# Performance work log

Hardware: AMD Instinct MI355X
Metric: run time of the kernel (lower is better)

The kernel has to match this reference:

```python
import jax, jax.numpy as jnp
import numpy as np

N = 40000
E = 640000
D_IN = 128
D_H = 128
D_OUT = 1


def setup_inputs() -> dict:
    key = jax.random.key(0)
    ks = jax.random.split(key, 10)
    s = 1.0 / np.sqrt(D_IN)
    sh = 1.0 / np.sqrt(D_H)
    return {
        "x": jax.random.normal(ks[0], (N, D_IN), dtype=jnp.float32),
        "edge_index": jax.random.randint(ks[1], (2, E), 0, N, dtype=jnp.int64),
        # conv1: lin_l (neighbors, has bias), lin_r (root, no bias)
        "W1l": jax.random.uniform(ks[2], (D_IN, D_H), jnp.float32, -s, s),
        "b1": jnp.zeros((D_H,), jnp.float32),
        "W1r": jax.random.uniform(ks[3], (D_IN, D_H), jnp.float32, -s, s),
        # conv2
        "W2l": jax.random.uniform(ks[4], (D_H, D_H), jnp.float32, -sh, sh),
        "b2": jnp.zeros((D_H,), jnp.float32),
        "W2r": jax.random.uniform(ks[5], (D_H, D_H), jnp.float32, -sh, sh),
        # final linear
        "Wo": jax.random.uniform(ks[6], (D_H, D_OUT), jnp.float32, -sh, sh),
        "bo": jnp.zeros((D_OUT,), jnp.float32),
    }


def _mean_aggregate(x, src, dst, num_nodes):
    # mean over incoming edges per target node (PyG SAGEConv default aggr='mean')
    msg_sum = jax.ops.segment_sum(x[src], dst, num_segments=num_nodes)  # [N, D]
    deg = jax.ops.segment_sum(jnp.ones((src.shape[0],), x.dtype), dst,
                              num_segments=num_nodes)
    return msg_sum / jnp.maximum(deg, 1.0)[:, None]


def _sage_conv(x, src, dst, Wl, b, Wr):
    # out = lin_l(mean_agg(neighbors)) + lin_r(x)
    agg = _mean_aggregate(x, src, dst, x.shape[0])
    return agg @ Wl + b + x @ Wr


def reference(x, edge_index, W1l, b1, W1r, W2l, b2, W2r, Wo, bo):
    src, dst = edge_index[0], edge_index[1]
    h = jax.nn.relu(_sage_conv(x, src, dst, W1l, b1, W1r))
    h = jax.nn.relu(_sage_conv(h, src, dst, W2l, b2, W2r))
    return h @ Wo + bo
```

## Files before the change

### kernel.cpp

```cpp
#include <hip/hip_runtime.h>
#include <hip/hip_bf16.h>


#define DH 128

typedef __attribute__((ext_vector_type(8))) short bf16x8;
typedef __attribute__((ext_vector_type(4))) float f32x4;

__device__ __forceinline__ unsigned short f2bf_rne(float f) {
    unsigned int u = __float_as_uint(f);
    return (unsigned short)((u + 0x7FFFu + ((u >> 16) & 1u)) >> 16);
}
__device__ __forceinline__ float bf2f(unsigned short h) {
    return __uint_as_float(((unsigned int)h) << 16);
}
__device__ __forceinline__ float bflo(unsigned int u) {
    return __uint_as_float(u << 16);
}
__device__ __forceinline__ float bfhi(unsigned int u) {
    return __uint_as_float(u & 0xffff0000u);
}


__global__ void deg_kernel(const int* __restrict__ dst, int* __restrict__ deg, int E) {
    int i = blockIdx.x * blockDim.x + threadIdx.x;
    if (i < E) atomicAdd(&deg[dst[i]], 1);
}

__global__ __launch_bounds__(256) void scan1_kernel(
    const int* __restrict__ deg, int* __restrict__ offs, int* __restrict__ bsum, int N)
{
    __shared__ int tmp[256];
    int tid = threadIdx.x;
    int i = blockIdx.x * 256 + tid;
    int v = (i < N) ? deg[i] : 0;
    tmp[tid] = v;
    __syncthreads();
    #pragma unroll
    for (int off = 1; off < 256; off <<= 1) {
        int t = (tid >= off) ? tmp[tid - off] : 0;
        __syncthreads();
        tmp[tid] += t;
        __syncthreads();
    }
    if (i < N) offs[i] = tmp[tid] - v;
    if (tid == 255) bsum[blockIdx.x] = tmp[255];
}

__global__ __launch_bounds__(256) void scan2_kernel(
    const int* __restrict__ bsum, int* __restrict__ boffs, int nb)
{
    __shared__ int tmp[256];
    int tid = threadIdx.x;
    int v = (tid < nb) ? bsum[tid] : 0;
    tmp[tid] = v;
    __syncthreads();
    #pragma unroll
    for (int off = 1; off < 256; off <<= 1) {
        int t = (tid >= off) ? tmp[tid - off] : 0;
        __syncthreads();
        tmp[tid] += t;
        __syncthreads();
    }
    if (tid < nb) boffs[tid] = tmp[tid] - v;
}

__global__ void fill_kernel(const int* __restrict__ src, const int* __restrict__ dst,
                            const int* __restrict__ offs, const int* __restrict__ boffs,
                            int* __restrict__ cursor, int* __restrict__ csr, int E)
{
    int e = blockIdx.x * blockDim.x + threadIdx.x;
    if (e >= E) return;
    int d = dst[e];
    int pos = atomicAdd(&cursor[d], 1);
    csr[offs[d] + boffs[d >> 8] + pos] = src[e];
}


__global__ __launch_bounds__(256) void tobf_kernel(
    const float* __restrict__ in, unsigned short* __restrict__ out, int n4)
{
    int i = blockIdx.x * 256 + threadIdx.x;
    if (i >= n4) return;
    float4 v = ((const float4*)in)[i];
    ushort4 o;
    o.x = f2bf_rne(v.x); o.y = f2bf_rne(v.y);
    o.z = f2bf_rne(v.z); o.w = f2bf_rne(v.w);
    ((ushort4*)out)[i] = o;
}


__global__ __launch_bounds__(256) void wprep_kernel(
    const float* __restrict__ W1l, const float* __restrict__ W1r,
    const float* __restrict__ W2l, const float* __restrict__ W2r,
    unsigned short* __restrict__ whi, unsigned short* __restrict__ wlo)
{
    int tid = blockIdx.x * 256 + threadIdx.x;
    if (tid >= 2 * 8 * 8 * 64) return;
    int lane = tid & 63;
    int f = (tid >> 6) & 7;
    int t = (tid >> 9) & 7;
    int conv = tid >> 12;
    const float* Wl = conv ? W2l : W1l;
    const float* Wr = conv ? W2r : W1r;
    int c = f * 16 + (lane & 15);
    int kb = t * 32 + (lane >> 4) * 8;
    size_t off = (size_t)tid * 8;
    #pragma unroll
    for (int j = 0; j < 8; ++j) {
        int k = kb + j;
        float w = (k < 128) ? Wl[k * 128 + c] : Wr[(k - 128) * 128 + c];
        unsigned short h = f2bf_rne(w);
        whi[off + j] = h;
        wlo[off + j] = f2bf_rne(w - bf2f(h));
    }
}


__global__ __launch_bounds__(256) void gather_mean_kernel(
    const unsigned short* __restrict__ featbf, const int* __restrict__ csr,
    const int* __restrict__ offs, const int* __restrict__ boffs,
    const int* __restrict__ deg, float* __restrict__ out, int N)
{
    int node = blockIdx.x * 4 + (threadIdx.x >> 6);
    if (node >= N) return;
    int lane = threadIdx.x & 63;
    int c = lane & 31;
    int half = lane >> 5;

    int start = offs[node] + boffs[node >> 8];
    int dg = deg[node];
    int end = start + dg;

    float4 a0 = make_float4(0.f, 0.f, 0.f, 0.f);
    float4 a1 = make_float4(0.f, 0.f, 0.f, 0.f);
    int e = start + half;
    for (; e + 2 < end; e += 4) {
        int s0 = csr[e], s1 = csr[e + 2];
        uint2 v0 = *(const uint2*)&featbf[(size_t)s0 * DH + c * 4];
        uint2 v1 = *(const uint2*)&featbf[(size_t)s1 * DH + c * 4];
        a0.x += bflo(v0.x); a0.y += bfhi(v0.x);
        a0.z += bflo(v0.y); a0.w += bfhi(v0.y);
        a1.x += bflo(v1.x); a1.y += bfhi(v1.x);
        a1.z += bflo(v1.y); a1.w += bfhi(v1.y);
    }
    if (e < end) {
        uint2 v0 = *(const uint2*)&featbf[(size_t)csr[e] * DH + c * 4];
        a0.x += bflo(v0.x); a0.y += bfhi(v0.x);
        a0.z += bflo(v0.y); a0.w += bfhi(v0.y);
    }
    a0.x += a1.x; a0.y += a1.y; a0.z += a1.z; a0.w += a1.w;
    a0.x += __shfl_down(a0.x, 32);
    a0.y += __shfl_down(a0.y, 32);
    a0.z += __shfl_down(a0.z, 32);
    a0.w += __shfl_down(a0.w, 32);
    if (half == 0) {
        float sc = 1.0f / (float)max(dg, 1);
        a0.x *= sc; a0.y *= sc; a0.z *= sc; a0.w *= sc;
        *(float4*)&out[(size_t)node * DH + c * 4] = a0;
    }
}


template<int HEAD>
__global__ __launch_bounds__(256) void sage_mfma_kernel(
    const float* __restrict__ Agg, const float* __restrict__ X,
    const unsigned short* __restrict__ whi, const unsigned short* __restrict__ wlo,
    const float* __restrict__ bias,
    float* __restrict__ Hf, unsigned short* __restrict__ Hbf,
    const float* __restrict__ Wo, const float* __restrict__ bo,
    float* __restrict__ outp)
{
    const int l = threadIdx.x & 63;
    const int wv = threadIdx.x >> 6;
    const int row0 = blockIdx.x * 64 + wv * 16;
    const int r = l & 15;
    const int kq = l >> 4;

    f32x4 acc[8];
    #pragma unroll
    for (int f = 0; f < 8; ++f) {
        float b = bias[f * 16 + r];
        acc[f] = (f32x4){b, b, b, b};
    }

    #pragma unroll
    for (int t = 0; t < 8; ++t) {
        const float* A = (t < 4) ? Agg : X;
        const float* ap = &A[(size_t)(row0 + r) * DH + (t & 3) * 32 + kq * 8];
        float4 f0 = *(const float4*)ap;
        float4 f1 = *(const float4*)(ap + 4);
        float a[8] = {f0.x, f0.y, f0.z, f0.w, f1.x, f1.y, f1.z, f1.w};
        bf16x8 ahi, alo;
        #pragma unroll
        for (int j = 0; j < 8; ++j) {
            unsigned short h = f2bf_rne(a[j]);
            ahi[j] = (short)h;
            alo[j] = (short)f2bf_rne(a[j] - bf2f(h));
        }
        const unsigned short* bh = whi + ((size_t)(t * 8) * 64 + l) * 8;
        const unsigned short* bl = wlo + ((size_t)(t * 8) * 64 + l) * 8;
        #pragma unroll
        for (int f = 0; f < 8; ++f) {
            bf16x8 bhi = *(const bf16x8*)(bh + (size_t)f * 64 * 8);
            bf16x8 blo = *(const bf16x8*)(bl + (size_t)f * 64 * 8);
            acc[f] = __builtin_amdgcn_mfma_f32_16x16x32_bf16(ahi, bhi, acc[f], 0, 0, 0);
            acc[f] = __builtin_amdgcn_mfma_f32_16x16x32_bf16(alo, bhi, acc[f], 0, 0, 0);
            acc[f] = __builtin_amdgcn_mfma_f32_16x16x32_bf16(ahi, blo, acc[f], 0, 0, 0);
        }
    }

    if (HEAD == 0) {
        #pragma unroll
        for (int f = 0; f < 8; ++f) {
            int col = f * 16 + r;
            #pragma unroll
            for (int q = 0; q < 4; ++q) {
                int row = row0 + kq * 4 + q;
                float v = fmaxf(acc[f][q], 0.0f);
                Hf[(size_t)row * DH + col] = v;
                Hbf[(size_t)row * DH + col] = f2bf_rne(v);
            }
        }
    } else {
        float wo[8];
        #pragma unroll
        for (int f = 0; f < 8; ++f) wo[f] = Wo[f * 16 + r];
        float s[4] = {0.f, 0.f, 0.f, 0.f};
        #pragma unroll
        for (int f = 0; f < 8; ++f)
            #pragma unroll
            for (int q = 0; q < 4; ++q)
                s[q] += fmaxf(acc[f][q], 0.0f) * wo[f];
        #pragma unroll
        for (int m = 1; m < 16; m <<= 1) {
            s[0] += __shfl_xor(s[0], m);
            s[1] += __shfl_xor(s[1], m);
            s[2] += __shfl_xor(s[2], m);
            s[3] += __shfl_xor(s[3], m);
        }
        if (r < 4) outp[row0 + kq * 4 + r] = s[r] + bo[0];
    }
}

extern "C" void kernel_launch(void* const* d_in, const int* in_sizes, int n_in,
                              void* d_out, int out_size, void* d_ws, size_t ws_size,
                              hipStream_t stream) {
    const float* x   = (const float*)d_in[0];
    const int*   ei  = (const int*)d_in[1];
    const float* W1l = (const float*)d_in[2];
    const float* b1  = (const float*)d_in[3];
    const float* W1r = (const float*)d_in[4];
    const float* W2l = (const float*)d_in[5];
    const float* b2  = (const float*)d_in[6];
    const float* W2r = (const float*)d_in[7];
    const float* Wo  = (const float*)d_in[8];
    const float* bo  = (const float*)d_in[9];
    float* out = (float*)d_out;

    const int N = in_sizes[0] / DH;
    const int E = in_sizes[1] / 2;
    const int* src = ei;
    const int* dst = ei + E;
    const int nb = (N + 255) / 256;

    float* agg = (float*)d_ws;
    float* h1  = agg + (size_t)N * DH;
    unsigned short* xbf  = (unsigned short*)(h1 + (size_t)N * DH);
    unsigned short* h1bf = xbf + (size_t)N * DH;
    int* deg    = (int*)(h1bf + (size_t)N * DH);
    int* offs   = deg + N;
    int* cursor = offs + N;
    int* bsum   = cursor + N;
    int* boffs  = bsum + 256;
    int* csr    = boffs + 256;
    unsigned short* whi = (unsigned short*)(csr + E);
    unsigned short* wlo = whi + 2 * 32768;

    hipMemsetAsync(deg, 0, (size_t)N * sizeof(int), stream);
    hipMemsetAsync(cursor, 0, (size_t)N * sizeof(int), stream);
    deg_kernel<<<(E + 255) / 256, 256, 0, stream>>>(dst, deg, E);
    tobf_kernel<<<(N * DH / 4 + 255) / 256, 256, 0, stream>>>(x, xbf, N * DH / 4);
    wprep_kernel<<<32, 256, 0, stream>>>(W1l, W1r, W2l, W2r, whi, wlo);
    scan1_kernel<<<nb, 256, 0, stream>>>(deg, offs, bsum, N);
    scan2_kernel<<<1, 256, 0, stream>>>(bsum, boffs, nb);
    fill_kernel<<<(E + 255) / 256, 256, 0, stream>>>(src, dst, offs, boffs, cursor, csr, E);

    gather_mean_kernel<<<(N + 3) / 4, 256, 0, stream>>>(xbf, csr, offs, boffs, deg, agg, N);
    sage_mfma_kernel<0><<<N / 64, 256, 0, stream>>>(
        agg, x, whi, wlo, b1, h1, h1bf, nullptr, nullptr, nullptr);

    gather_mean_kernel<<<(N + 3) / 4, 256, 0, stream>>>(h1bf, csr, offs, boffs, deg, agg, N);
    sage_mfma_kernel<1><<<N / 64, 256, 0, stream>>>(
        agg, h1, whi + 32768, wlo + 32768, b2, nullptr, nullptr, Wo, bo, out);
}
```

Before: 259.6 us.

## Store activations as bf16 hi/lo pairs, fuse prep kernels, double rows per MFMA wave

Merges the degree count, x conversion and weight prep into one prep kernel and folds the two memsets into one, cutting launches. The gather kernel now writes the aggregate as bf16 hi/lo split arrays, so the MFMA kernel loads pre-split operands instead of fp32 and re-splitting. Layer 1 writes H as hi/lo too. Each wave now handles two 16-row tiles so weight fragments are reused across 32 rows, and the gather loop is unrolled to 4 outstanding loads per half-wave. The aggregate hi part is truncated rather than rounded, which can shift numerics slightly, and the doubled accumulators raise register pressure.

```diff
diff --git a/kernel.cpp b/kernel.cpp
--- a/kernel.cpp
+++ b/kernel.cpp
@@ -22,10 +22,55 @@
 }
 
 
-__global__ void deg_kernel(const int* __restrict__ dst, int* __restrict__ deg, int E) {
-    int i = blockIdx.x * blockDim.x + threadIdx.x;
-    if (i < E) atomicAdd(&deg[dst[i]], 1);
-}
+__global__ __launch_bounds__(256) void prep_kernel(
+    const float* __restrict__ x,
+    unsigned short* __restrict__ xhi, unsigned short* __restrict__ xlo,
+    const int* __restrict__ dst, int* __restrict__ deg,
+    const float* __restrict__ W1l, const float* __restrict__ W1r,
+    const float* __restrict__ W2l, const float* __restrict__ W2r,
+    unsigned short* __restrict__ whi, unsigned short* __restrict__ wlo,
+    int n4, int E, int nbA, int nbB)
+{
+    int b = blockIdx.x;
+    if (b < nbA) {
+        int i = b * 256 + threadIdx.x;
+        if (i >= n4) return;
+        float4 v = ((const float4*)x)[i];
+        unsigned short hx = f2bf_rne(v.x), hy = f2bf_rne(v.y);
+        unsigned short hz = f2bf_rne(v.z), hw = f2bf_rne(v.w);
+        uint2 hi, lo;
+        hi.x = ((unsigned)hy << 16) | hx;
+        hi.y = ((unsigned)hw << 16) | hz;
+        lo.x = ((unsigned)f2bf_rne(v.y - bf2f(hy)) << 16) | f2bf_rne(v.x - bf2f(hx));
+        lo.y = ((unsigned)f2bf_rne(v.w - bf2f(hw)) << 16) | f2bf_rne(v.z - bf2f(hz));
+        ((uint2*)xhi)[i] = hi;
+        ((uint2*)xlo)[i] = lo;
+    } else if (b < nbA + nbB) {
+        int i = (b - nbA) * 256 + threadIdx.x;
+        if (i < E) atomicAdd(&deg[dst[i]], 1);
+    } else {
+        int tid = (b - nbA - nbB) * 256 + threadIdx.x;
+        if (tid >= 2 * 8 * 8 * 64) return;
+        int lane = tid & 63;
+        int f = (tid >> 6) & 7;
+        int t = (tid >> 9) & 7;
+        int conv = tid >> 12;
+        const float* Wl = conv ? W2l : W1l;
+        const float* Wr = conv ? W2r : W1r;
+        int c = f * 16 + (lane & 15);
+        int kb = t * 32 + (lane >> 4) * 8;
+        size_t off = (size_t)tid * 8;
+        #pragma unroll
+        for (int j = 0; j < 8; ++j) {
+            int k = kb + j;
+            float w = (k < 128) ? Wl[k * 128 + c] : Wr[(k - 128) * 128 + c];
+            unsigned short h = f2bf_rne(w);
+            whi[off + j] = h;
+            wlo[off + j] = f2bf_rne(w - bf2f(h));
+        }
+    }
+}
+
 
 __global__ __launch_bounds__(256) void scan1_kernel(
     const int* __restrict__ deg, int* __restrict__ offs, int* __restrict__ bsum, int N)
@@ -77,50 +122,11 @@
 }
 
 
-__global__ __launch_bounds__(256) void tobf_kernel(
-    const float* __restrict__ in, unsigned short* __restrict__ out, int n4)
-{
-    int i = blockIdx.x * 256 + threadIdx.x;
-    if (i >= n4) return;
-    float4 v = ((const float4*)in)[i];
-    ushort4 o;
-    o.x = f2bf_rne(v.x); o.y = f2bf_rne(v.y);
-    o.z = f2bf_rne(v.z); o.w = f2bf_rne(v.w);
-    ((ushort4*)out)[i] = o;
-}
-
-
-__global__ __launch_bounds__(256) void wprep_kernel(
-    const float* __restrict__ W1l, const float* __restrict__ W1r,
-    const float* __restrict__ W2l, const float* __restrict__ W2r,
-    unsigned short* __restrict__ whi, unsigned short* __restrict__ wlo)
-{
-    int tid = blockIdx.x * 256 + threadIdx.x;
-    if (tid >= 2 * 8 * 8 * 64) return;
-    int lane = tid & 63;
-    int f = (tid >> 6) & 7;
-    int t = (tid >> 9) & 7;
-    int conv = tid >> 12;
-    const float* Wl = conv ? W2l : W1l;
-    const float* Wr = conv ? W2r : W1r;
-    int c = f * 16 + (lane & 15);
-    int kb = t * 32 + (lane >> 4) * 8;
-    size_t off = (size_t)tid * 8;
-    #pragma unroll
-    for (int j = 0; j < 8; ++j) {
-        int k = kb + j;
-        float w = (k < 128) ? Wl[k * 128 + c] : Wr[(k - 128) * 128 + c];
-        unsigned short h = f2bf_rne(w);
-        whi[off + j] = h;
-        wlo[off + j] = f2bf_rne(w - bf2f(h));
-    }
-}
-
-
 __global__ __launch_bounds__(256) void gather_mean_kernel(
     const unsigned short* __restrict__ featbf, const int* __restrict__ csr,
     const int* __restrict__ offs, const int* __restrict__ boffs,
-    const int* __restrict__ deg, float* __restrict__ out, int N)
+    const int* __restrict__ deg,
+    unsigned short* __restrict__ outhi, unsigned short* __restrict__ outlo, int N)
 {
     int node = blockIdx.x * 4 + (threadIdx.x >> 6);
     if (node >= N) return;
@@ -132,24 +138,27 @@
     int dg = deg[node];
     int end = start + dg;
 
-    float4 a0 = make_float4(0.f, 0.f, 0.f, 0.f);
-    float4 a1 = make_float4(0.f, 0.f, 0.f, 0.f);
+    float4 a0 = make_float4(0.f,0.f,0.f,0.f), a1 = a0, a2 = a0, a3 = a0;
     int e = start + half;
-    for (; e + 2 < end; e += 4) {
-        int s0 = csr[e], s1 = csr[e + 2];
+    for (; e + 6 < end; e += 8) {
+        int s0 = csr[e], s1 = csr[e + 2], s2 = csr[e + 4], s3 = csr[e + 6];
         uint2 v0 = *(const uint2*)&featbf[(size_t)s0 * DH + c * 4];
         uint2 v1 = *(const uint2*)&featbf[(size_t)s1 * DH + c * 4];
-        a0.x += bflo(v0.x); a0.y += bfhi(v0.x);
-        a0.z += bflo(v0.y); a0.w += bfhi(v0.y);
-        a1.x += bflo(v1.x); a1.y += bfhi(v1.x);
-        a1.z += bflo(v1.y); a1.w += bfhi(v1.y);
-    }
-    if (e < end) {
-        uint2 v0 = *(const uint2*)&featbf[(size_t)csr[e] * DH + c * 4];
-        a0.x += bflo(v0.x); a0.y += bfhi(v0.x);
-        a0.z += bflo(v0.y); a0.w += bfhi(v0.y);
-    }
-    a0.x += a1.x; a0.y += a1.y; a0.z += a1.z; a0.w += a1.w;
+        uint2 v2 = *(const uint2*)&featbf[(size_t)s2 * DH + c * 4];
+        uint2 v3 = *(const uint2*)&featbf[(size_t)s3 * DH + c * 4];
+        a0.x += bflo(v0.x); a0.y += bfhi(v0.x); a0.z += bflo(v0.y); a0.w += bfhi(v0.y);
+        a1.x += bflo(v1.x); a1.y += bfhi(v1.x); a1.z += bflo(v1.y); a1.w += bfhi(v1.y);
+        a2.x += bflo(v2.x); a2.y += bfhi(v2.x); a2.z += bflo(v2.y); a2.w += bfhi(v2.y);
+        a3.x += bflo(v3.x); a3.y += bfhi(v3.x); a3.z += bflo(v3.y); a3.w += bfhi(v3.y);
+    }
+    for (; e < end; e += 2) {
+        uint2 v = *(const uint2*)&featbf[(size_t)csr[e] * DH + c * 4];
+        a0.x += bflo(v.x); a0.y += bfhi(v.x); a0.z += bflo(v.y); a0.w += bfhi(v.y);
+    }
+    a0.x += a1.x + a2.x + a3.x;
+    a0.y += a1.y + a2.y + a3.y;
+    a0.z += a1.z + a2.z + a3.z;
+    a0.w += a1.w + a2.w + a3.w;
     a0.x += __shfl_down(a0.x, 32);
     a0.y += __shfl_down(a0.y, 32);
     a0.z += __shfl_down(a0.z, 32);
@@ -157,89 +166,118 @@
     if (half == 0) {
         float sc = 1.0f / (float)max(dg, 1);
         a0.x *= sc; a0.y *= sc; a0.z *= sc; a0.w *= sc;
-        *(float4*)&out[(size_t)node * DH + c * 4] = a0;
+        unsigned int ux = __float_as_uint(a0.x), uy = __float_as_uint(a0.y);
+        unsigned int uz = __float_as_uint(a0.z), uw = __float_as_uint(a0.w);
+        uint2 hi;
+        hi.x = (uy & 0xffff0000u) | (ux >> 16);
+        hi.y = (uw & 0xffff0000u) | (uz >> 16);
+        uint2 lo;
+        lo.x = ((unsigned)f2bf_rne(a0.y - __uint_as_float(uy & 0xffff0000u)) << 16)
+             | f2bf_rne(a0.x - __uint_as_float(ux & 0xffff0000u));
+        lo.y = ((unsigned)f2bf_rne(a0.w - __uint_as_float(uw & 0xffff0000u)) << 16)
+             | f2bf_rne(a0.z - __uint_as_float(uz & 0xffff0000u));
+        *(uint2*)&outhi[(size_t)node * DH + c * 4] = hi;
+        *(uint2*)&outlo[(size_t)node * DH + c * 4] = lo;
     }
 }
 
 
 template<int HEAD>
 __global__ __launch_bounds__(256) void sage_mfma_kernel(
-    const float* __restrict__ Agg, const float* __restrict__ X,
+    const unsigned short* __restrict__ agghi, const unsigned short* __restrict__ agglo,
+    const unsigned short* __restrict__ xhi, const unsigned short* __restrict__ xlo,
     const unsigned short* __restrict__ whi, const unsigned short* __restrict__ wlo,
     const float* __restrict__ bias,
-    float* __restrict__ Hf, unsigned short* __restrict__ Hbf,
+    unsigned short* __restrict__ Hhi, unsigned short* __restrict__ Hlo,
     const float* __restrict__ Wo, const float* __restrict__ bo,
-    float* __restrict__ outp)
+    float* __restrict__ outp, int N)
 {
     const int l = threadIdx.x & 63;
     const int wv = threadIdx.x >> 6;
-    const int row0 = blockIdx.x * 64 + wv * 16;
     const int r = l & 15;
     const int kq = l >> 4;
-
-    f32x4 acc[8];
+    const int base0 = blockIdx.x * 128 + wv * 16;
+    const int base1 = base0 + 64;
+    const bool v1 = (base1 + 16 <= N);
+
+    f32x4 acc0[8], acc1[8];
     #pragma unroll
     for (int f = 0; f < 8; ++f) {
         float b = bias[f * 16 + r];
-        acc[f] = (f32x4){b, b, b, b};
+        acc0[f] = (f32x4){b, b, b, b};
+        acc1[f] = (f32x4){b, b, b, b};
     }
 
     #pragma unroll
     for (int t = 0; t < 8; ++t) {
-        const float* A = (t < 4) ? Agg : X;
-        const float* ap = &A[(size_t)(row0 + r) * DH + (t & 3) * 32 + kq * 8];
-        float4 f0 = *(const float4*)ap;
-        float4 f1 = *(const float4*)(ap + 4);
-        float a[8] = {f0.x, f0.y, f0.z, f0.w, f1.x, f1.y, f1.z, f1.w};
-        bf16x8 ahi, alo;
-        #pragma unroll
-        for (int j = 0; j < 8; ++j) {
-            unsigned short h = f2bf_rne(a[j]);
-            ahi[j] = (short)h;
-            alo[j] = (short)f2bf_rne(a[j] - bf2f(h));
+        const unsigned short* Ah = (t < 4) ? agghi : xhi;
+        const unsigned short* Al = (t < 4) ? agglo : xlo;
+        size_t ao0 = (size_t)(base0 + r) * DH + (t & 3) * 32 + kq * 8;
+        bf16x8 a0h = *(const bf16x8*)&Ah[ao0];
+        bf16x8 a0l = *(const bf16x8*)&Al[ao0];
+        bf16x8 a1h = {0,0,0,0,0,0,0,0};
+        bf16x8 a1l = {0,0,0,0,0,0,0,0};
+        if (v1) {
+            size_t ao1 = ao0 + (size_t)64 * DH;
+            a1h = *(const bf16x8*)&Ah[ao1];
+            a1l = *(const bf16x8*)&Al[ao1];
         }
         const unsigned short* bh = whi + ((size_t)(t * 8) * 64 + l) * 8;
         const unsigned short* bl = wlo + ((size_t)(t * 8) * 64 + l) * 8;
         #pragma unroll
         for (int f = 0; f < 8; ++f) {
-            bf16x8 bhi = *(const bf16x8*)(bh + (size_t)f * 64 * 8);
-            bf16x8 blo = *(const bf16x8*)(bl + (size_t)f * 64 * 8);
-            acc[f] = __builtin_amdgcn_mfma_f32_16x16x32_bf16(ahi, bhi, acc[f], 0, 0, 0);
-            acc[f] = __builtin_amdgcn_mfma_f32_16x16x32_bf16(alo, bhi, acc[f], 0, 0, 0);
-            acc[f] = __builtin_amdgcn_mfma_f32_16x16x32_bf16(ahi, blo, acc[f], 0, 0, 0);
+            bf16x8 bhi = *(const bf16x8*)(bh + (size_t)f * 512);
+            bf16x8 blo = *(const bf16x8*)(bl + (size_t)f * 512);
+            acc0[f] = __builtin_amdgcn_mfma_f32_16x16x32_bf16(a0h, bhi, acc0[f], 0, 0, 0);
+            acc0[f] = __builtin_amdgcn_mfma_f32_16x16x32_bf16(a0l, bhi, acc0[f], 0, 0, 0);
+            acc0[f] = __builtin_amdgcn_mfma_f32_16x16x32_bf16(a0h, blo, acc0[f], 0, 0, 0);
+            acc1[f] = __builtin_amdgcn_mfma_f32_16x16x32_bf16(a1h, bhi, acc1[f], 0, 0, 0);
+            acc1[f] = __builtin_amdgcn_mfma_f32_16x16x32_bf16(a1l, bhi, acc1[f], 0, 0, 0);
+            acc1[f] = __builtin_amdgcn_mfma_f32_16x16x32_bf16(a1h, blo, acc1[f], 0, 0, 0);
         }
     }
 
     if (HEAD == 0) {
         #pragma unroll
-        for (int f = 0; f < 8; ++f) {
-            int col = f * 16 + r;
+        for (int rg = 0; rg < 2; ++rg) {
+            if (rg == 1 && !v1) break;
+            int base = rg ? base1 : base0;
             #pragma unroll
-            for (int q = 0; q < 4; ++q) {
-                int row = row0 + kq * 4 + q;
-                float v = fmaxf(acc[f][q], 0.0f);
-                Hf[(size_t)row * DH + col] = v;
-                Hbf[(size_t)row * DH + col] = f2bf_rne(v);
+            for (int f = 0; f < 8; ++f) {
+                int col = f * 16 + r;
+                #pragma unroll
+                for (int q = 0; q < 4; ++q) {
+                    float v = fmaxf(rg ? acc1[f][q] : acc0[f][q], 0.0f);
+                    size_t idx = (size_t)(base + kq * 4 + q) * DH + col;
+                    unsigned short h = f2bf_rne(v);
+                    Hhi[idx] = h;
+                    Hlo[idx] = f2bf_rne(v - bf2f(h));
+                }
             }
         }
     } else {
         float wo[8];
         #pragma unroll
         for (int f = 0; f < 8; ++f) wo[f] = Wo[f * 16 + r];
-        float s[4] = {0.f, 0.f, 0.f, 0.f};
-        #pragma unroll
-        for (int f = 0; f < 8; ++f)
+        #pragma unroll
+        for (int rg = 0; rg < 2; ++rg) {
+            if (rg == 1 && !v1) break;
+            int base = rg ? base1 : base0;
+            float s[4] = {0.f, 0.f, 0.f, 0.f};
             #pragma unroll
-            for (int q = 0; q < 4; ++q)
-                s[q] += fmaxf(acc[f][q], 0.0f) * wo[f];
-        #pragma unroll
-        for (int m = 1; m < 16; m <<= 1) {
-            s[0] += __shfl_xor(s[0], m);
-            s[1] += __shfl_xor(s[1], m);
-            s[2] += __shfl_xor(s[2], m);
-            s[3] += __shfl_xor(s[3], m);
-        }
-        if (r < 4) outp[row0 + kq * 4 + r] = s[r] + bo[0];
+            for (int f = 0; f < 8; ++f)
+                #pragma unroll
+                for (int q = 0; q < 4; ++q)
+                    s[q] += fmaxf(rg ? acc1[f][q] : acc0[f][q], 0.0f) * wo[f];
+            #pragma unroll
+            for (int m = 1; m < 16; m <<= 1) {
+                s[0] += __shfl_xor(s[0], m);
+                s[1] += __shfl_xor(s[1], m);
+                s[2] += __shfl_xor(s[2], m);
+                s[3] += __shfl_xor(s[3], m);
+            }
+            if (r < 4) outp[base + kq * 4 + r] = s[r] + bo[0];
+        }
     }
 }
 
@@ -263,34 +301,44 @@
     const int* src = ei;
     const int* dst = ei + E;
     const int nb = (N + 255) / 256;
-
-    float* agg = (float*)d_ws;
-    float* h1  = agg + (size_t)N * DH;
-    unsigned short* xbf  = (unsigned short*)(h1 + (size_t)N * DH);
-    unsigned short* h1bf = xbf + (size_t)N * DH;
-    int* deg    = (int*)(h1bf + (size_t)N * DH);
-    int* offs   = deg + N;
-    int* cursor = offs + N;
-    int* bsum   = cursor + N;
+    const size_t NDH = (size_t)N * DH;
+    const int n4 = N * DH / 4;
+    const int nbA = (n4 + 255) / 256;
+    const int nbB = (E + 255) / 256;
+
+    unsigned short* xhi   = (unsigned short*)d_ws;
+    unsigned short* xlo   = xhi + NDH;
+    unsigned short* h1hi  = xlo + NDH;
+    unsigned short* h1lo  = h1hi + NDH;
+    unsigned short* agghi = h1lo + NDH;
+    unsigned short* agglo = agghi + NDH;
+    unsigned short* whi   = agglo + NDH;
+    unsigned short* wlo   = whi + 65536;
+    int* deg    = (int*)(wlo + 65536);
+    int* cursor = deg + N;
+    int* offs   = cursor + N;
+    int* bsum   = offs + N;
     int* boffs  = bsum + 256;
     int* csr    = boffs + 256;
-    unsigned short* whi = (unsigned short*)(csr + E);
-    unsigned short* wlo = whi + 2 * 32768;
-
-    hipMemsetAsync(deg, 0, (size_t)N * sizeof(int), stream);
-    hipMemsetAsync(cursor, 0, (size_t)N * sizeof(int), stream);
-    deg_kernel<<<(E + 255) / 256, 256, 0, stream>>>(dst, deg, E);
-    tobf_kernel<<<(N * DH / 4 + 255) / 256, 256, 0, stream>>>(x, xbf, N * DH / 4);
-    wprep_kernel<<<32, 256, 0, stream>>>(W1l, W1r, W2l, W2r, whi, wlo);
+
+    hipMemsetAsync(deg, 0, 2 * (size_t)N * sizeof(int), stream);
+    prep_kernel<<<nbA + nbB + 32, 256, 0, stream>>>(
+        x, xhi, xlo, dst, deg, W1l, W1r, W2l, W2r, whi, wlo, n4, E, nbA, nbB);
     scan1_kernel<<<nb, 256, 0, stream>>>(deg, offs, bsum, N);
     scan2_kernel<<<1, 256, 0, stream>>>(bsum, boffs, nb);
-    fill_kernel<<<(E + 255) / 256, 256, 0, stream>>>(src, dst, offs, boffs, cursor, csr, E);
-
-    gather_mean_kernel<<<(N + 3) / 4, 256, 0, stream>>>(xbf, csr, offs, boffs, deg, agg, N);
-    sage_mfma_kernel<0><<<N / 64, 256, 0, stream>>>(
-        agg, x, whi, wlo, b1, h1, h1bf, nullptr, nullptr, nullptr);
-
-    gather_mean_kernel<<<(N + 3) / 4, 256, 0, stream>>>(h1bf, csr, offs, boffs, deg, agg, N);
-    sage_mfma_kernel<1><<<N / 64, 256, 0, stream>>>(
-        agg, h1, whi + 32768, wlo + 32768, b2, nullptr, nullptr, Wo, bo, out);
-}
+    fill_kernel<<<nbB, 256, 0, stream>>>(src, dst, offs, boffs, cursor, csr, E);
+
+    const int convGrid = (N + 127) / 128;
+
+    gather_mean_kernel<<<(N + 3) / 4, 256, 0, stream>>>(
+        xhi, csr, offs, boffs, deg, agghi, agglo, N);
+    sage_mfma_kernel<0><<<convGrid, 256, 0, stream>>>(
+        agghi, agglo, xhi, xlo, whi, wlo, b1, h1hi, h1lo,
+        nullptr, nullptr, nullptr, N);
+
+    gather_mean_kernel<<<(N + 3) / 4, 256, 0, stream>>>(
+        h1hi, csr, offs, boffs, deg, agghi, agglo, N);
+    sage_mfma_kernel<1><<<convGrid, 256, 0, stream>>>(
+        agghi, agglo, h1hi, h1lo, whi + 32768, wlo + 32768, b2, nullptr, nullptr,
+        Wo, bo, out, N);
+}
```

Result: no change. 258.0 us (-0.6%).
